# Performance work log

Measured on AMD Instinct MI355X. Metric: run time of the kernel, lower is better.

The kernel has to match this reference:

```python
import jax, jax.numpy as jnp
import numpy as np
import math

POOL_H = 8
POOL_W = 16
LATENT_H = 48
LATENT_W = 80
VISUAL_LEN = 7680   # 2 frames of 48*80 latent tokens
SPARSITY = 0.9
NUM_HEADS = 16
HEAD_DIM = 64


def _reorg_restore():
    # part/block/sub-block token reorganization so pooled sub-blocks are contiguous
    part = LATENT_W * POOL_H          # 640
    blk = LATENT_W                    # 80
    sub = POOL_W                      # 16
    bpp = part // blk                 # blocks per part = 8
    spb = blk // sub                  # sub-blocks per block = 5
    # orig index = b*blk + c*sub + i ; new order iterates (c, b, i)
    pat = np.arange(part).reshape(bpp, spb, sub).transpose(1, 0, 2).reshape(-1)
    nparts = VISUAL_LEN // part
    reorg = (np.arange(nparts)[:, None] * part + pat[None, :]).reshape(-1)
    restore = np.argsort(reorg)       # inverse permutation
    return jnp.asarray(reorg), jnp.asarray(restore)

REORG_IDX, RESTORE_IDX = _reorg_restore()


def _draft_attn_map(q, k):
    # q, k: [L, H, D] -> pooled attention map [H, S, S]
    L, H, D = q.shape
    nf = L // (LATENT_H * LATENT_W)
    def pool(x):
        # 2D avg-pool each frame (dims divide exactly -> reshape+mean)
        x = x.reshape(nf, LATENT_H // POOL_H, POOL_H, LATENT_W // POOL_W, POOL_W, H, D)
        return x.mean(axis=(2, 4)).reshape(-1, H, D)   # [S, H, D]
    qs, ks = pool(q), pool(k)
    scores = jnp.einsum('lhd,mhd->hlm', qs, ks) / math.sqrt(D)
    return jax.nn.softmax(scores, axis=-1)


def _percentile_mask(attn, r):
    # keep top-r fraction of entries per head: threshold = max of k smallest
    H, S, _ = attn.shape
    n = S * S
    kk = int((1.0 - r) * n)           # number of entries dropped (0 < kk < n here)
    thr = jnp.sort(attn.reshape(H, n), axis=-1)[:, kk - 1]
    return attn >= thr[:, None, None]


def _head_attn(qh, kh, vh, mblk):
    # qh/kh/vh: [L, D]; mblk: [nb, nb] bool block mask, block size L//nb (=128)
    L, D = qh.shape
    nb = mblk.shape[0]
    mB = L // nb
    s = (qh @ kh.T) * (1.0 / math.sqrt(D))              # [L, L]
    s = jnp.where(mblk[:, None, :, None], s.reshape(nb, mB, nb, mB), -jnp.inf)
    s = s.reshape(L, L)
    m = jnp.max(s, axis=-1, keepdims=True)
    m = jnp.where(jnp.isfinite(m), m, 0.0)              # fully-masked rows -> 0 output
    p = jnp.exp(s - m)                                  # exp(-inf) = 0
    p = p / jnp.maximum(p.sum(-1, keepdims=True), 1e-30)
    return p @ vh


def _forward(q, k, v, batch_size, max_seqlen_q):
    attn = _draft_attn_map(q, k)                        # [H, S, S]
    mask = _percentile_mask(attn, 1.0 - SPARSITY)       # [H, S, S] bool
    qr, kr, vr = q[REORG_IDX], k[REORG_IDX], v[REORG_IDX]
    qh = jnp.swapaxes(qr, 0, 1)                         # [H, L, D]
    kh = jnp.swapaxes(kr, 0, 1)
    vh = jnp.swapaxes(vr, 0, 1)
    f = jax.checkpoint(lambda t: _head_attn(*t))
    out = jax.lax.map(f, (qh, kh, vh, mask))            # sequential over heads: [H, L, D]
    x = jnp.swapaxes(out, 0, 1)[RESTORE_IDX]            # [L, H, D]
    return x.reshape(batch_size, max_seqlen_q, q.shape[1], q.shape[2])


def setup_inputs() -> dict:
    key = jax.random.key(0)
    kq, kk, kv = jax.random.split(key, 3)
    L = VISUAL_LEN
    q = jax.random.normal(kq, (L, NUM_HEADS, HEAD_DIM), dtype=jnp.float32)
    k = jax.random.normal(kk, (L, NUM_HEADS, HEAD_DIM), dtype=jnp.float32)
    v = jax.random.normal(kv, (L, NUM_HEADS, HEAD_DIM), dtype=jnp.float32)
    return {
        'q': q, 'k': k, 'v': v,
        'cu_seqlens_q': jnp.array([0, L], dtype=jnp.int32),
        'cu_seqlens_kv': jnp.array([0, L], dtype=jnp.int32),
        'max_seqlen_q': L,
        'max_seqlen_kv': L,
        'batch_size': 1,
    }


def reference(q, k, v, cu_seqlens_q, cu_seqlens_kv, max_seqlen_q, max_seqlen_kv, batch_size):
    return _forward(q, k, v, batch_size, max_seqlen_q)
```

## Files before the change

kernel.cpp:

```cpp
#include <hip/hip_runtime.h>

#define L_TOK   7680
#define NHEAD   16
#define HDIM    64
#define NBLK    60
#define KEEP    361
#define QS_OFF   0u
#define KS_OFF   491520u
#define CNT_OFF  983040u
#define COL_OFF  986880u
#define KHM_OFF  1217280u
#define VTM_OFF  16945920u
#define ORD_OFF  32674560u

typedef short bf16x8 __attribute__((ext_vector_type(8)));
typedef short bf16x4 __attribute__((ext_vector_type(4)));
typedef float f32x4  __attribute__((ext_vector_type(4)));

__device__ __forceinline__ unsigned int cvtpk(float lo, float hi) {
  unsigned int r;
  asm("v_cvt_pk_bf16_f32 %0, %1, %2" : "=v"(r) : "v"(lo), "v"(hi));
  return r;
}

__device__ __forceinline__ f32x4 mfma16(bf16x4 a, bf16x4 b, f32x4 c) {
#if __has_builtin(__builtin_amdgcn_mfma_f32_16x16x16bf16_1k)
  return __builtin_amdgcn_mfma_f32_16x16x16bf16_1k(a, b, c, 0, 0, 0);
#else
  asm("v_mfma_f32_16x16x16_bf16 %0, %1, %2, %0" : "+v"(c) : "v"(a), "v"(b));
  return c;
#endif
}

__device__ __forceinline__ void gll16(const unsigned short* gsrc, unsigned short* ldst) {
  __builtin_amdgcn_global_load_lds(
      (const __attribute__((address_space(1))) unsigned int*)gsrc,
      (__attribute__((address_space(3))) unsigned int*)ldst, 16, 0, 0);
}

__global__ __launch_bounds__(256) void prep_kernel(
    const float* __restrict__ qin, const float* __restrict__ kin,
    const float* __restrict__ vin, double* __restrict__ qs, double* __restrict__ ks,
    unsigned short* __restrict__ khm, unsigned short* __restrict__ vtm) {
  __shared__ float stg[128 * 68];
  __shared__ double psum[4][64];
  const int h = blockIdx.x, blk = blockIdx.y, t = threadIdx.x;
  const int p = blk / 5, c = blk % 5;
  const int q4 = t >> 6, dq = t & 63;

  unsigned short* kdst = khm + (size_t)(h * 60 + blk) * 8192;
  #pragma unroll
  for (int it = 0; it < 4; ++it) {
    int sidx = it * 256 + t;  int row = sidx >> 3, s = sidx & 7;
    int tok = p * 640 + (row >> 4) * 80 + c * 16 + (row & 15);
    const float* src = kin + (size_t)tok * 1024 + h * 64 + s * 8;
    float4 a = ((const float4*)src)[0], b = ((const float4*)src)[1];
    uint4 un; un.x = cvtpk(a.x, a.y); un.y = cvtpk(a.z, a.w);
    un.z = cvtpk(b.x, b.y); un.w = cvtpk(b.z, b.w);
    *(uint4*)(kdst + row * 64 + ((s ^ (row & 7)) * 8)) = un;
    *(float4*)&stg[row * 68 + s * 8] = a;
    *(float4*)&stg[row * 68 + s * 8 + 4] = b;
  }
  __syncthreads();
  { double ka = 0.0;
    for (int r = 0; r < 32; ++r) ka += (double)stg[(q4 * 32 + r) * 68 + dq];
    psum[q4][dq] = ka; }
  __syncthreads();
  if (t < 64)
    ks[(size_t)(h * 60 + blk) * 64 + t] =
        (psum[0][t] + psum[1][t] + psum[2][t] + psum[3][t]) * (1.0 / 128.0);

  #pragma unroll
  for (int it = 0; it < 8; ++it) {
    int idx = it * 256 + t;  int row = idx >> 4, f4 = idx & 15;
    int tok = p * 640 + (row >> 4) * 80 + c * 16 + (row & 15);
    float4 a = ((const float4*)(vin + (size_t)tok * 1024 + h * 64))[f4];
    *(float4*)&stg[row * 68 + f4 * 4] = a;
  }
  double a0 = 0, a1 = 0, a2 = 0, a3 = 0;
  #pragma unroll
  for (int i = 0; i < 32; i += 4) {
    #pragma unroll
    for (int j2 = 0; j2 < 4; ++j2) {
      int row = q4 * 32 + i + j2;
      int tok = p * 640 + (row >> 4) * 80 + c * 16 + (row & 15);
      double v = (double)qin[(size_t)tok * 1024 + h * 64 + dq];
      if (j2 == 0) a0 += v; else if (j2 == 1) a1 += v;
      else if (j2 == 2) a2 += v; else a3 += v;
    }
  }
  __syncthreads();
  psum[q4][dq] = (a0 + a1) + (a2 + a3);
  __syncthreads();
  if (t < 64)
    qs[(size_t)(h * 60 + blk) * 64 + t] =
        (psum[0][t] + psum[1][t] + psum[2][t] + psum[3][t]) * (1.0 / 128.0);

  unsigned short* vdst = vtm + (size_t)(h * 60 + blk) * 8192;
  #pragma unroll
  for (int it = 0; it < 4; ++it) {
    int u = it * 256 + t;  int d = u >> 4, sl = u & 15;
    int half = sl >> 3, slot = sl & 7;
    int kbase = half * 64 + (slot >> 2) * 32 + (slot & 3) * 4;
    uint4 un;
    un.x = cvtpk(stg[(kbase + 0) * 68 + d],  stg[(kbase + 1) * 68 + d]);
    un.y = cvtpk(stg[(kbase + 2) * 68 + d],  stg[(kbase + 3) * 68 + d]);
    un.z = cvtpk(stg[(kbase + 16) * 68 + d], stg[(kbase + 17) * 68 + d]);
    un.w = cvtpk(stg[(kbase + 18) * 68 + d], stg[(kbase + 19) * 68 + d]);
    *(uint4*)(vdst + half * 4096 + d * 64 + ((slot ^ (d & 7)) * 8)) = un;
  }
}

__global__ void scores_kernel(const double* __restrict__ qs, const double* __restrict__ ks,
                              float* __restrict__ probsF) {
  const int i = blockIdx.x, h = blockIdx.y, j = threadIdx.x;
  const double* qr = qs + (size_t)(h * 60 + i) * 64;
  double sc = -1.0e300;
  if (j < 60) {
    const double* kr = ks + (size_t)(h * 60 + j) * 64;
    double a0 = 0, a1 = 0, a2 = 0, a3 = 0;
    #pragma unroll
    for (int d = 0; d < 64; d += 4) {
      a0 += qr[d]     * kr[d];
      a1 += qr[d + 1] * kr[d + 1];
      a2 += qr[d + 2] * kr[d + 2];
      a3 += qr[d + 3] * kr[d + 3];
    }
    sc = ((a0 + a1) + (a2 + a3)) * 0.125;
  }
  double m = sc;
  #pragma unroll
  for (int o = 32; o; o >>= 1) m = fmax(m, __shfl_xor(m, o, 64));
  double e = (j < 60) ? exp(sc - m) : 0.0;
  double ssum = e;
  #pragma unroll
  for (int o = 32; o; o >>= 1) ssum += __shfl_xor(ssum, o, 64);
  if (j < 60) probsF[(size_t)(h * 60 + i) * 60 + j] = (float)(e / ssum);
}

__global__ __launch_bounds__(256) void select_kernel(const float* __restrict__ probsF,
                                                     int* __restrict__ counts,
                                                     int* __restrict__ cols,
                                                     int* __restrict__ order) {
  const int h = blockIdx.x, t = threadIdx.x;
  __shared__ float pb[3600];
  __shared__ int hist[2048];
  __shared__ int warr[4];
  __shared__ int sh_digit, sh_above;
  __shared__ int scnt[60];

  unsigned int myv[15];
  #pragma unroll
  for (int m2 = 0; m2 < 15; ++m2) {
    int i = t + m2 * 256;
    float v = 0.0f;
    if (i < 3600) { v = probsF[(size_t)h * 3600 + i]; pb[i] = v; }
    myv[m2] = __float_as_uint(v);
  }
  __syncthreads();

  unsigned int prefix = 0;
  int rank = KEEP;
  const int lane = t & 63, w = t >> 6;
  #pragma unroll
  for (int pass = 0; pass < 3; ++pass) {
    const int shift = (pass == 0) ? 21 : (pass == 1) ? 10 : 0;
    const int width = (pass == 2) ? 10 : 11;
    const int dmask = (1 << width) - 1;
    for (int i = t; i < 2048; i += 256) hist[i] = 0;
    __syncthreads();
    const int hb = shift + width;
    #pragma unroll
    for (int m2 = 0; m2 < 15; ++m2) {
      unsigned int u = myv[m2];
      if (u && (pass == 0 || (u >> hb) == (prefix >> hb)))
        atomicAdd(&hist[(int)((u >> shift) & dmask)], 1);
    }
    __syncthreads();
    const int base = t * 8;
    int bcnt[8], s = 0;
    #pragma unroll
    for (int b = 0; b < 8; ++b) { bcnt[b] = hist[base + b]; s += bcnt[b]; }
    int incl = s;
    #pragma unroll
    for (int o = 1; o < 64; o <<= 1) {
      int y = __shfl_down(incl, o, 64);
      if (lane + o < 64) incl += y;
    }
    if (lane == 0) warr[w] = incl;
    __syncthreads();
    int above_w = 0;
    for (int w2 = w + 1; w2 < 4; ++w2) above_w += warr[w2];
    int run = (incl - s) + above_w;
    #pragma unroll
    for (int b = 7; b >= 0; --b) {
      int c = bcnt[b];
      if (c > 0 && run < rank && run + c >= rank) { sh_digit = base + b; sh_above = run; }
      run += c;
    }
    __syncthreads();
    prefix |= ((unsigned int)sh_digit) << shift;
    rank -= sh_above;
    __syncthreads();
  }

  const float thr = __uint_as_float(prefix);
  if (t < 60) {
    int cnt = 0;
    int tmp[60];
    for (int j = 0; j < 60; ++j)
      if (pb[t * 60 + j] >= thr) tmp[cnt++] = j;
    for (int j = 0; j < cnt; ++j) cols[(size_t)(h * 60 + t) * 60 + j] = tmp[j];
    counts[h * 60 + t] = cnt;
    scnt[t] = cnt;
  }
  __syncthreads();
  if (t < 60) {
    int c = scnt[t], rk = 0;
    for (int j = 0; j < 60; ++j) {
      int cj = scnt[j];
      rk += (cj > c) || (cj == c && j < t);
    }
    order[h * 60 + rk] = t;
  }
}

__global__ __launch_bounds__(256, 3) void attn_kernel(
    const float* __restrict__ qin, const unsigned short* __restrict__ khm,
    const unsigned short* __restrict__ vtm, const int* __restrict__ counts,
    const int* __restrict__ cols, const int* __restrict__ order,
    float* __restrict__ out) {
  const int h = blockIdx.x;
  const int qb = order[h * 60 + blockIdx.y];
  const int t = threadIdx.x, w = t >> 6, lane = t & 63;
  const int g = lane >> 4, n = lane & 15, sw = n & 7;
  __shared__ __align__(16) unsigned short LDSb[24576];
  #define KT(b) (LDSb + (b) * 8192)
  #define VT(b) (LDSb + (b) * 8192 + 4096)

  const int cnt = counts[h * 60 + qb];
  const int pq = qb / 5, cq = qb % 5;
  if (cnt == 0) {
    for (int i = t; i < 2048; i += 256) {
      int row = i >> 4, f4 = i & 15;
      int tok = pq * 640 + (row >> 4) * 80 + cq * 16 + (row & 15);
      float4 z = {0.f, 0.f, 0.f, 0.f};
      *(float4*)(out + (size_t)tok * 1024 + h * 64 + f4 * 4) = z;
    }
    return;
  }

  const int* mycols = cols + (size_t)(h * 60 + qb) * 60;
  int colv = mycols[lane < cnt ? lane : 0];

  const float C2 = 0.18033688011112042f;
  bf16x8 aq[2][2];
  #pragma unroll
  for (int qt = 0; qt < 2; ++qt) {
    int lq = w * 32 + qt * 16 + n;
    int tok = pq * 640 + (lq >> 4) * 80 + cq * 16 + (lq & 15);
    const float* qrow = qin + (size_t)tok * 1024 + h * 64;
    #pragma unroll
    for (int hh = 0; hh < 2; ++hh) {
      const float4* s4 = (const float4*)(qrow + hh * 32 + g * 8);
      float4 a = s4[0], b2 = s4[1];
      union { bf16x8 v; unsigned int uw[4]; } un;
      un.uw[0] = cvtpk(a.x * C2, a.y * C2);   un.uw[1] = cvtpk(a.z * C2, a.w * C2);
      un.uw[2] = cvtpk(b2.x * C2, b2.y * C2); un.uw[3] = cvtpk(b2.z * C2, b2.w * C2);
      aq[qt][hh] = un.v;
    }
  }

  const f32x4 zero4 = {0.f, 0.f, 0.f, 0.f};
  f32x4 acco[2][4];
  float lst[2] = {0.f, 0.f};
  #pragma unroll
  for (int qt = 0; qt < 2; ++qt)
    #pragma unroll
    for (int dt = 0; dt < 4; ++dt) acco[qt][dt] = zero4;

  const unsigned short* khm_h = khm + (size_t)(h * 60) * 8192;
  const unsigned short* vtm_h = vtm + (size_t)(h * 60) * 8192;
  const int nht = cnt * 2;

  {
    int kb0 = __shfl(colv, 0, 64);
    asm volatile("s_waitcnt vmcnt(0)" ::: "memory");
    const unsigned short* ksrc = khm_h + (size_t)kb0 * 8192;
    const unsigned short* vsrc = vtm_h + (size_t)kb0 * 8192;
    #pragma unroll
    for (int j = 0; j < 2; ++j) {
      gll16(ksrc + (size_t)((w * 2 + j) * 512) + lane * 8, KT(0) + (w * 2 + j) * 512);
      gll16(vsrc + (size_t)((w * 2 + j) * 512) + lane * 8, VT(0) + (w * 2 + j) * 512);
    }
  }

  int b = 0;
  for (int ht = 0; ht < nht; ++ht) {
    const int bn = (b == 2) ? 0 : b + 1;
    if (ht + 1 < nht) {
      int kbn = __shfl(colv, (ht + 1) >> 1, 64);
      int hof = ((ht + 1) & 1) * 4096;
      const unsigned short* ksrc = khm_h + (size_t)kbn * 8192 + hof;
      const unsigned short* vsrc = vtm_h + (size_t)kbn * 8192 + hof;
      #pragma unroll
      for (int j = 0; j < 2; ++j) {
        gll16(ksrc + (size_t)((w * 2 + j) * 512) + lane * 8, KT(bn) + (w * 2 + j) * 512);
        gll16(vsrc + (size_t)((w * 2 + j) * 512) + lane * 8, VT(bn) + (w * 2 + j) * 512);
      }
      asm volatile("s_waitcnt vmcnt(4)" ::: "memory");
    } else {
      asm volatile("s_waitcnt vmcnt(0)" ::: "memory");
    }
    __syncthreads();

    f32x4 accs[2][4];
    #pragma unroll
    for (int qt = 0; qt < 2; ++qt)
      #pragma unroll
      for (int kt = 0; kt < 4; ++kt) accs[qt][kt] = zero4;
    __builtin_amdgcn_s_setprio(1);
    #pragma unroll
    for (int kt = 0; kt < 4; ++kt) {
      int rowbase = (kt * 16 + n) * 64;
      bf16x8 k0 = *(const bf16x8*)&KT(b)[rowbase + ((g ^ sw) * 8)];
      bf16x8 k1 = *(const bf16x8*)&KT(b)[rowbase + (((4 + g) ^ sw) * 8)];
      accs[0][kt] = __builtin_amdgcn_mfma_f32_16x16x32_bf16(k0, aq[0][0], accs[0][kt], 0, 0, 0);
      accs[0][kt] = __builtin_amdgcn_mfma_f32_16x16x32_bf16(k1, aq[0][1], accs[0][kt], 0, 0, 0);
      accs[1][kt] = __builtin_amdgcn_mfma_f32_16x16x32_bf16(k0, aq[1][0], accs[1][kt], 0, 0, 0);
      accs[1][kt] = __builtin_amdgcn_mfma_f32_16x16x32_bf16(k1, aq[1][1], accs[1][kt], 0, 0, 0);
    }
    __builtin_amdgcn_s_setprio(0);

    bf16x4 pbv[2][4];
    #pragma unroll
    for (int qt = 0; qt < 2; ++qt) {
      float rs0 = 0.f, rs1 = 0.f, rs2 = 0.f, rs3 = 0.f;
      #pragma unroll
      for (int kt = 0; kt < 4; ++kt) {
        float p0 = __builtin_amdgcn_exp2f(accs[qt][kt][0]);
        float p1 = __builtin_amdgcn_exp2f(accs[qt][kt][1]);
        float p2 = __builtin_amdgcn_exp2f(accs[qt][kt][2]);
        float p3 = __builtin_amdgcn_exp2f(accs[qt][kt][3]);
        rs0 += p0; rs1 += p1; rs2 += p2; rs3 += p3;
        union { unsigned int u[2]; bf16x4 v; } pb;
        pb.u[0] = cvtpk(p0, p1);
        pb.u[1] = cvtpk(p2, p3);
        pbv[qt][kt] = pb.v;
      }
      lst[qt] += (rs0 + rs1) + (rs2 + rs3);
    }

    __builtin_amdgcn_s_setprio(1);
    #pragma unroll
    for (int kp = 0; kp < 2; ++kp) {
      #pragma unroll
      for (int dt = 0; dt < 4; ++dt) {
        int d = dt * 16 + n;
        bf16x8 vv = *(const bf16x8*)&VT(b)[d * 64 + (((kp * 4 + g) ^ sw) * 8)];
        bf16x4 vlo = __builtin_shufflevector(vv, vv, 0, 1, 2, 3);
        bf16x4 vhi = __builtin_shufflevector(vv, vv, 4, 5, 6, 7);
        acco[0][dt] = mfma16(vlo, pbv[0][2 * kp],     acco[0][dt]);
        acco[0][dt] = mfma16(vhi, pbv[0][2 * kp + 1], acco[0][dt]);
        acco[1][dt] = mfma16(vlo, pbv[1][2 * kp],     acco[1][dt]);
        acco[1][dt] = mfma16(vhi, pbv[1][2 * kp + 1], acco[1][dt]);
      }
    }
    __builtin_amdgcn_s_setprio(0);
    b = bn;
  }

  __syncthreads();
  float* Ot = (float*)LDSb;
  #pragma unroll
  for (int qt = 0; qt < 2; ++qt) {
    float l = lst[qt];
    l += __shfl_xor(l, 16, 64);
    l += __shfl_xor(l, 32, 64);
    float inv = 1.0f / l;
    int q = w * 32 + qt * 16 + n;
    #pragma unroll
    for (int dt = 0; dt < 4; ++dt)
      #pragma unroll
      for (int r = 0; r < 4; ++r)
        Ot[q * 68 + dt * 16 + 4 * g + r] = acco[qt][dt][r] * inv;
  }
  __syncthreads();
  for (int i = t; i < 2048; i += 256) {
    int q = i >> 4, f4 = i & 15;
    int tok = pq * 640 + (q >> 4) * 80 + cq * 16 + (q & 15);
    float4 val = *(float4*)&Ot[q * 68 + f4 * 4];
    *(float4*)(out + (size_t)tok * 1024 + h * 64 + f4 * 4) = val;
  }
  #undef KT
  #undef VT
}

extern "C" void kernel_launch(void* const* d_in, const int* in_sizes, int n_in,
                              void* d_out, int out_size, void* d_ws, size_t ws_size,
                              hipStream_t stream) {
  const float* qin = (const float*)d_in[0];
  const float* kin = (const float*)d_in[1];
  const float* vin = (const float*)d_in[2];
  char* ws = (char*)d_ws;
  double* qs = (double*)(ws + QS_OFF);
  double* ks = (double*)(ws + KS_OFF);
  int* counts = (int*)(ws + CNT_OFF);
  int* cols = (int*)(ws + COL_OFF);
  float* probsF = (float*)(ws + COL_OFF);
  unsigned short* khm = (unsigned short*)(ws + KHM_OFF);
  unsigned short* vtm = (unsigned short*)(ws + VTM_OFF);
  int* order = (int*)(ws + ORD_OFF);
  float* outp = (float*)d_out;

  prep_kernel<<<dim3(16, 60), 256, 0, stream>>>(qin, kin, vin, qs, ks, khm, vtm);
  scores_kernel<<<dim3(60, 16), 64, 0, stream>>>(qs, ks, probsF);
  select_kernel<<<16, 256, 0, stream>>>(probsF, counts, cols, order);
  attn_kernel<<<dim3(16, 60), 256, 0, stream>>>(qin, khm, vtm, counts, cols, order, outp);
}
```

Before: 88.77 us.

## Deepen K/V prefetch to two tiles ahead in triple-buffered attention loop

Changes the attention main loop's software pipeline from prefetch-distance one to two. Two K/V half-tiles are now loaded before the loop, and each iteration issues the load for tile ht+2 into the third buffer after the barrier. This gives global-to-LDS loads more time to complete before they are consumed, and moving the issue after the barrier avoids overwriting a buffer still being read. It also drops a temporary array in the mask-column extraction and writes columns directly to global memory. The tradeoff is more in-flight loads per wave, and the unchanged vmcnt(4) wait count now has to match the deeper pipeline.

```diff
diff --git a/kernel.cpp b/kernel.cpp
--- a/kernel.cpp
+++ b/kernel.cpp
@@ -207,10 +207,8 @@
   const float thr = __uint_as_float(prefix);
   if (t < 60) {
     int cnt = 0;
-    int tmp[60];
     for (int j = 0; j < 60; ++j)
-      if (pb[t * 60 + j] >= thr) tmp[cnt++] = j;
-    for (int j = 0; j < cnt; ++j) cols[(size_t)(h * 60 + t) * 60 + j] = tmp[j];
+      if (pb[t * 60 + j] >= thr) cols[(size_t)(h * 60 + t) * 60 + (cnt++)] = j;
     counts[h * 60 + t] = cnt;
     scnt[t] = cnt;
   }
@@ -293,27 +291,39 @@
       gll16(ksrc + (size_t)((w * 2 + j) * 512) + lane * 8, KT(0) + (w * 2 + j) * 512);
       gll16(vsrc + (size_t)((w * 2 + j) * 512) + lane * 8, VT(0) + (w * 2 + j) * 512);
     }
-  }
-
-  int b = 0;
+    if (nht > 1) {
+      const unsigned short* ksrc1 = ksrc + 4096;
+      const unsigned short* vsrc1 = vsrc + 4096;
+      #pragma unroll
+      for (int j = 0; j < 2; ++j) {
+        gll16(ksrc1 + (size_t)((w * 2 + j) * 512) + lane * 8, KT(1) + (w * 2 + j) * 512);
+        gll16(vsrc1 + (size_t)((w * 2 + j) * 512) + lane * 8, VT(1) + (w * 2 + j) * 512);
+      }
+    }
+  }
+
+  int bb = 0;
   for (int ht = 0; ht < nht; ++ht) {
-    const int bn = (b == 2) ? 0 : b + 1;
     if (ht + 1 < nht) {
-      int kbn = __shfl(colv, (ht + 1) >> 1, 64);
-      int hof = ((ht + 1) & 1) * 4096;
-      const unsigned short* ksrc = khm_h + (size_t)kbn * 8192 + hof;
-      const unsigned short* vsrc = vtm_h + (size_t)kbn * 8192 + hof;
-      #pragma unroll
-      for (int j = 0; j < 2; ++j) {
-        gll16(ksrc + (size_t)((w * 2 + j) * 512) + lane * 8, KT(bn) + (w * 2 + j) * 512);
-        gll16(vsrc + (size_t)((w * 2 + j) * 512) + lane * 8, VT(bn) + (w * 2 + j) * 512);
-      }
       asm volatile("s_waitcnt vmcnt(4)" ::: "memory");
     } else {
       asm volatile("s_waitcnt vmcnt(0)" ::: "memory");
     }
     __syncthreads();
 
+    if (ht + 2 < nht) {
+      int b2 = bb + 2; if (b2 >= 3) b2 -= 3;
+      int kbn = __shfl(colv, (ht + 2) >> 1, 64);
+      int hof = ((ht + 2) & 1) * 4096;
+      const unsigned short* ksrc = khm_h + (size_t)kbn * 8192 + hof;
+      const unsigned short* vsrc = vtm_h + (size_t)kbn * 8192 + hof;
+      #pragma unroll
+      for (int j = 0; j < 2; ++j) {
+        gll16(ksrc + (size_t)((w * 2 + j) * 512) + lane * 8, KT(b2) + (w * 2 + j) * 512);
+        gll16(vsrc + (size_t)((w * 2 + j) * 512) + lane * 8, VT(b2) + (w * 2 + j) * 512);
+      }
+    }
+
     f32x4 accs[2][4];
     #pragma unroll
     for (int qt = 0; qt < 2; ++qt)
@@ -323,8 +333,8 @@
     #pragma unroll
     for (int kt = 0; kt < 4; ++kt) {
       int rowbase = (kt * 16 + n) * 64;
-      bf16x8 k0 = *(const bf16x8*)&KT(b)[rowbase + ((g ^ sw) * 8)];
-      bf16x8 k1 = *(const bf16x8*)&KT(b)[rowbase + (((4 + g) ^ sw) * 8)];
+      bf16x8 k0 = *(const bf16x8*)&KT(bb)[rowbase + ((g ^ sw) * 8)];
+      bf16x8 k1 = *(const bf16x8*)&KT(bb)[rowbase + (((4 + g) ^ sw) * 8)];
       accs[0][kt] = __builtin_amdgcn_mfma_f32_16x16x32_bf16(k0, aq[0][0], accs[0][kt], 0, 0, 0);
       accs[0][kt] = __builtin_amdgcn_mfma_f32_16x16x32_bf16(k1, aq[0][1], accs[0][kt], 0, 0, 0);
       accs[1][kt] = __builtin_amdgcn_mfma_f32_16x16x32_bf16(k0, aq[1][0], accs[1][kt], 0, 0, 0);
@@ -357,7 +367,7 @@
       #pragma unroll
       for (int dt = 0; dt < 4; ++dt) {
         int d = dt * 16 + n;
-        bf16x8 vv = *(const bf16x8*)&VT(b)[d * 64 + (((kp * 4 + g) ^ sw) * 8)];
+        bf16x8 vv = *(const bf16x8*)&VT(bb)[d * 64 + (((kp * 4 + g) ^ sw) * 8)];
         bf16x4 vlo = __builtin_shufflevector(vv, vv, 0, 1, 2, 3);
         bf16x4 vhi = __builtin_shufflevector(vv, vv, 4, 5, 6, 7);
         acco[0][dt] = mfma16(vlo, pbv[0][2 * kp],     acco[0][dt]);
@@ -367,7 +377,7 @@
       }
     }
     __builtin_amdgcn_s_setprio(0);
-    b = bn;
+    bb = (bb == 2) ? 0 : bb + 1;
   }
 
   __syncthreads();
```

Measured after the change: 84.86 us. -4.4%, faster.

## Split each KV block across two wave groups with 512-thread attention blocks

Applied to the files above, without the earlier changes.

The attention kernel now launches 512 threads per block. Two groups of four waves each process one half of every 128-token KV block, and their partial outputs and row sums are combined through LDS at the end. The pipeline changes from triple-buffered half-tiles to double-buffered full tiles, with a full vmcnt(0) wait and a barrier at each step. The select kernel also writes selected columns directly instead of going through a local temp array. The aim is more waves in flight and fewer loop iterations, at the cost of a larger LDS footprint, a reduction step, and less load/compute overlap.

```diff
diff --git a/kernel.cpp b/kernel.cpp
--- a/kernel.cpp
+++ b/kernel.cpp
@@ -207,10 +207,8 @@
   const float thr = __uint_as_float(prefix);
   if (t < 60) {
     int cnt = 0;
-    int tmp[60];
     for (int j = 0; j < 60; ++j)
-      if (pb[t * 60 + j] >= thr) tmp[cnt++] = j;
-    for (int j = 0; j < cnt; ++j) cols[(size_t)(h * 60 + t) * 60 + j] = tmp[j];
+      if (pb[t * 60 + j] >= thr) cols[(size_t)(h * 60 + t) * 60 + (cnt++)] = j;
     counts[h * 60 + t] = cnt;
     scnt[t] = cnt;
   }
@@ -225,7 +223,7 @@
   }
 }
 
-__global__ __launch_bounds__(256, 3) void attn_kernel(
+__global__ __launch_bounds__(512, 4) void attn_kernel(
     const float* __restrict__ qin, const unsigned short* __restrict__ khm,
     const unsigned short* __restrict__ vtm, const int* __restrict__ counts,
     const int* __restrict__ cols, const int* __restrict__ order,
@@ -234,14 +232,15 @@
   const int qb = order[h * 60 + blockIdx.y];
   const int t = threadIdx.x, w = t >> 6, lane = t & 63;
   const int g = lane >> 4, n = lane & 15, sw = n & 7;
-  __shared__ __align__(16) unsigned short LDSb[24576];
-  #define KT(b) (LDSb + (b) * 8192)
-  #define VT(b) (LDSb + (b) * 8192 + 4096)
+  const int grp = w >> 2, wq = w & 3;
+  __shared__ __align__(16) unsigned short LDSb[32768];
+  #define KT(b) (LDSb + (b) * 16384)
+  #define VT(b) (LDSb + (b) * 16384 + 8192)
 
   const int cnt = counts[h * 60 + qb];
   const int pq = qb / 5, cq = qb % 5;
   if (cnt == 0) {
-    for (int i = t; i < 2048; i += 256) {
+    for (int i = t; i < 2048; i += 512) {
       int row = i >> 4, f4 = i & 15;
       int tok = pq * 640 + (row >> 4) * 80 + cq * 16 + (row & 15);
       float4 z = {0.f, 0.f, 0.f, 0.f};
@@ -257,7 +256,7 @@
   bf16x8 aq[2][2];
   #pragma unroll
   for (int qt = 0; qt < 2; ++qt) {
-    int lq = w * 32 + qt * 16 + n;
+    int lq = wq * 32 + qt * 16 + n;
     int tok = pq * 640 + (lq >> 4) * 80 + cq * 16 + (lq & 15);
     const float* qrow = qin + (size_t)tok * 1024 + h * 64;
     #pragma unroll
@@ -281,7 +280,8 @@
 
   const unsigned short* khm_h = khm + (size_t)(h * 60) * 8192;
   const unsigned short* vtm_h = vtm + (size_t)(h * 60) * 8192;
-  const int nht = cnt * 2;
+  const int krow0 = grp * 64;
+  const int vhof  = grp * 4096;
 
   {
     int kb0 = __shfl(colv, 0, 64);
@@ -295,24 +295,21 @@
     }
   }
 
-  int b = 0;
-  for (int ht = 0; ht < nht; ++ht) {
-    const int bn = (b == 2) ? 0 : b + 1;
-    if (ht + 1 < nht) {
-      int kbn = __shfl(colv, (ht + 1) >> 1, 64);
-      int hof = ((ht + 1) & 1) * 4096;
-      const unsigned short* ksrc = khm_h + (size_t)kbn * 8192 + hof;
-      const unsigned short* vsrc = vtm_h + (size_t)kbn * 8192 + hof;
+  for (int ki = 0; ki < cnt; ++ki) {
+    const int b = ki & 1;
+    asm volatile("s_waitcnt vmcnt(0)" ::: "memory");
+    __syncthreads();
+
+    if (ki + 1 < cnt) {
+      int kbn = __shfl(colv, ki + 1, 64);
+      const unsigned short* ksrc = khm_h + (size_t)kbn * 8192;
+      const unsigned short* vsrc = vtm_h + (size_t)kbn * 8192;
       #pragma unroll
       for (int j = 0; j < 2; ++j) {
-        gll16(ksrc + (size_t)((w * 2 + j) * 512) + lane * 8, KT(bn) + (w * 2 + j) * 512);
-        gll16(vsrc + (size_t)((w * 2 + j) * 512) + lane * 8, VT(bn) + (w * 2 + j) * 512);
+        gll16(ksrc + (size_t)((w * 2 + j) * 512) + lane * 8, KT(b ^ 1) + (w * 2 + j) * 512);
+        gll16(vsrc + (size_t)((w * 2 + j) * 512) + lane * 8, VT(b ^ 1) + (w * 2 + j) * 512);
       }
-      asm volatile("s_waitcnt vmcnt(4)" ::: "memory");
-    } else {
-      asm volatile("s_waitcnt vmcnt(0)" ::: "memory");
-    }
-    __syncthreads();
+    }
 
     f32x4 accs[2][4];
     #pragma unroll
@@ -322,7 +319,7 @@
     __builtin_amdgcn_s_setprio(1);
     #pragma unroll
     for (int kt = 0; kt < 4; ++kt) {
-      int rowbase = (kt * 16 + n) * 64;
+      int rowbase = (krow0 + kt * 16 + n) * 64;
       bf16x8 k0 = *(const bf16x8*)&KT(b)[rowbase + ((g ^ sw) * 8)];
       bf16x8 k1 = *(const bf16x8*)&KT(b)[rowbase + (((4 + g) ^ sw) * 8)];
       accs[0][kt] = __builtin_amdgcn_mfma_f32_16x16x32_bf16(k0, aq[0][0], accs[0][kt], 0, 0, 0);
@@ -357,7 +354,7 @@
       #pragma unroll
       for (int dt = 0; dt < 4; ++dt) {
         int d = dt * 16 + n;
-        bf16x8 vv = *(const bf16x8*)&VT(b)[d * 64 + (((kp * 4 + g) ^ sw) * 8)];
+        bf16x8 vv = *(const bf16x8*)&VT(b)[vhof + d * 64 + (((kp * 4 + g) ^ sw) * 8)];
         bf16x4 vlo = __builtin_shufflevector(vv, vv, 0, 1, 2, 3);
         bf16x4 vhi = __builtin_shufflevector(vv, vv, 4, 5, 6, 7);
         acco[0][dt] = mfma16(vlo, pbv[0][2 * kp],     acco[0][dt]);
@@ -367,26 +364,45 @@
       }
     }
     __builtin_amdgcn_s_setprio(0);
-    b = bn;
-  }
-
+  }
+
+  asm volatile("s_waitcnt vmcnt(0)" ::: "memory");
   __syncthreads();
   float* Ot = (float*)LDSb;
+  float* Ls = (float*)LDSb + 8704;
   #pragma unroll
   for (int qt = 0; qt < 2; ++qt) {
     float l = lst[qt];
     l += __shfl_xor(l, 16, 64);
     l += __shfl_xor(l, 32, 64);
-    float inv = 1.0f / l;
-    int q = w * 32 + qt * 16 + n;
-    #pragma unroll
-    for (int dt = 0; dt < 4; ++dt)
-      #pragma unroll
-      for (int r = 0; r < 4; ++r)
-        Ot[q * 68 + dt * 16 + 4 * g + r] = acco[qt][dt][r] * inv;
-  }
-  __syncthreads();
-  for (int i = t; i < 2048; i += 256) {
+    int q = wq * 32 + qt * 16 + n;
+    if (grp == 0) {
+      #pragma unroll
+      for (int dt = 0; dt < 4; ++dt)
+        #pragma unroll
+        for (int r = 0; r < 4; ++r)
+          Ot[q * 68 + dt * 16 + 4 * g + r] = acco[qt][dt][r];
+      if (lane < 16) Ls[q] = l;
+    }
+    lst[qt] = l;
+  }
+  __syncthreads();
+  if (grp == 1) {
+    #pragma unroll
+    for (int qt = 0; qt < 2; ++qt) {
+      int q = wq * 32 + qt * 16 + n;
+      float inv = 1.0f / (Ls[q] + lst[qt]);
+      #pragma unroll
+      for (int dt = 0; dt < 4; ++dt)
+        #pragma unroll
+        for (int r = 0; r < 4; ++r) {
+          int idx = q * 68 + dt * 16 + 4 * g + r;
+          Ot[idx] = (Ot[idx] + acco[qt][dt][r]) * inv;
+        }
+    }
+  }
+  __syncthreads();
+  for (int i = t; i < 2048; i += 512) {
     int q = i >> 4, f4 = i & 15;
     int tok = pq * 640 + (q >> 4) * 80 + cq * 16 + (q & 15);
     float4 val = *(float4*)&Ot[q * 68 + f4 * 4];
@@ -416,5 +432,5 @@
   prep_kernel<<<dim3(16, 60), 256, 0, stream>>>(qin, kin, vin, qs, ks, khm, vtm);
   scores_kernel<<<dim3(60, 16), 64, 0, stream>>>(qs, ks, probsF);
   select_kernel<<<16, 256, 0, stream>>>(probsF, counts, cols, order);
-  attn_kernel<<<dim3(16, 60), 256, 0, stream>>>(qin, khm, vtm, counts, cols, order, outp);
-}
+  attn_kernel<<<dim3(16, 60), 512, 0, stream>>>(qin, khm, vtm, counts, cols, order, outp);
+}
```

Result: faster. 85.33 us, median of 2 (-3.9%).
